# Optimization experiments

Hardware: AMD Instinct MI355X
Metric: run time of the kernel (lower is better)

The kernel has to match this reference:

```python
import jax, jax.numpy as jnp
import numpy as np

N_NODES = 100000
N_EDGES = 3200000
F_IN, F_HID, F_OUT = 32, 32, 16


def spline_conv(x, edge_index, edge_attr, W, root, bias):
    """SplineConv, dim=1, kernel_size=2, degree=1, open spline, aggr='mean'.
    Basis weights over the 2 kernel slots are (1-u, u) for pseudo u in [0,1).
    W: [2, Fin, Fout], root: [Fin, Fout], bias: [Fout]."""
    src, dst = edge_index[0], edge_index[1]
    u = jnp.clip(edge_attr[:, 0:1], 0.0, 1.0)          # [E,1]
    x_src = x[src]                                      # [E,Fin] gather
    msg = (1.0 - u) * (x_src @ W[0]) + u * (x_src @ W[1])  # [E,Fout]
    agg = jax.ops.segment_sum(msg, dst, num_segments=x.shape[0])
    cnt = jax.ops.segment_sum(jnp.ones((msg.shape[0],), dtype=x.dtype), dst,
                              num_segments=x.shape[0])
    agg = agg / jnp.maximum(cnt, 1.0)[:, None]          # mean aggregation
    return agg + x @ root + bias


def setup_inputs() -> dict:
    key = jax.random.key(0)
    ks = jax.random.split(key, 9)
    x = jax.random.normal(ks[0], (N_NODES, F_IN), dtype=jnp.float32)
    edge_index = jax.random.randint(ks[1], (2, N_EDGES), 0, N_NODES, dtype=jnp.int64)
    edge_attr = jax.random.uniform(ks[2], (N_EDGES, 1), dtype=jnp.float32)
    s1 = 1.0 / np.sqrt(F_IN)
    s2 = 1.0 / np.sqrt(F_HID)
    W1 = jax.random.normal(ks[3], (2, F_IN, F_HID), dtype=jnp.float32) * s1
    root1 = jax.random.normal(ks[4], (F_IN, F_HID), dtype=jnp.float32) * s1
    b1 = jnp.zeros((F_HID,), dtype=jnp.float32)
    W2 = jax.random.normal(ks[5], (2, F_HID, F_OUT), dtype=jnp.float32) * s2
    root2 = jax.random.normal(ks[6], (F_HID, F_OUT), dtype=jnp.float32) * s2
    b2 = jnp.zeros((F_OUT,), dtype=jnp.float32)
    return {"x": x, "edge_index": edge_index, "edge_attr": edge_attr,
            "W1": W1, "root1": root1, "b1": b1,
            "W2": W2, "root2": root2, "b2": b2}


def reference(x, edge_index, edge_attr, W1, root1, b1, W2, root2, b2):
    # dropout is identity in eval mode
    h = jax.nn.relu(spline_conv(x, edge_index, edge_attr, W1, root1, b1))
    h = spline_conv(h, edge_index, edge_attr, W2, root2, b2)
    return jax.nn.log_softmax(h, axis=1)
```

## Files before the change

### kernel.cpp

```cpp
#include <hip/hip_runtime.h>
#include <math.h>

#define NN 100000
#define NE 3200000
#define BSH 6
#define BSZ 64
#define NBKT 1563
#define CAP 2560
#define STILE 8192
#define NTBS 391
#define NPB 1563
#define TST 68
#define NOFF (NBKT + 1)

#define FMA4(a, s, v) { (a).x += (s)*(v).x; (a).y += (s)*(v).y; (a).z += (s)*(v).z; (a).w += (s)*(v).w; }

typedef float v2f __attribute__((ext_vector_type(2)));

__device__ __forceinline__ unsigned fp8pack4(float a, float b, float c, float d) {
    int r = __builtin_amdgcn_cvt_pk_fp8_f32(a, b, 0, false);
    r = __builtin_amdgcn_cvt_pk_fp8_f32(c, d, r, true);
    return (unsigned)r;
}

#define LDE(pp, vv, idx) { int e_ = (idx); \
    if (e_ < cn) { pp = (unsigned)pks[cs + e_]; vv = x1[(size_t)(pp >> 15) * 8 + j]; } \
    else { pp = 0u; vv = 0u; } }
#define ACC(pp, vv) { float u_ = (float)((pp) & 511u) * (1.f / 511.f); \
    v2f lo_ = __builtin_amdgcn_cvt_pk_f32_fp8((vv), false); \
    v2f hi_ = __builtin_amdgcn_cvt_pk_f32_fp8((vv), true); \
    T0 += lo_.x; B0 += u_ * lo_.x;  T1 += lo_.y; B1 += u_ * lo_.y; \
    T2 += hi_.x; B2 += u_ * hi_.x;  T3 += hi_.y; B3 += u_ * hi_.y; }

__global__ __launch_bounds__(512) void sp_k(
    const int* __restrict__ ei, const float* __restrict__ ea,
    const float* __restrict__ x, const float* __restrict__ R, const float* __restrict__ b,
    int* __restrict__ pk, unsigned short* __restrict__ offs,
    unsigned* __restrict__ xb, float* __restrict__ xr)
{
    __shared__ __align__(16) union {
        struct { int h[2048]; int staged[STILE]; } sc;
        struct { float Rs[1024]; float xs[64 * 33]; } pp;
    } sm;
    int t = threadIdx.x;

    if (blockIdx.x < NTBS) {
        int* h = sm.sc.h;
        for (int i = t; i < 2048; i += 512) h[i] = 0;
        __syncthreads();
        int e0 = blockIdx.x * STILE;
        int cntblk = NE - e0; if (cntblk > STILE) cntblk = STILE;
        int dreg[16];
        #pragma unroll
        for (int i = 0; i < 16; i++) {
            int e = e0 + i * 512 + t;
            dreg[i] = -1;
            if (e < NE) {
                int d = ei[NE + e];
                dreg[i] = d;
                atomicAdd(&h[d >> BSH], 1);
            }
        }
        __syncthreads();
        int4 hc = ((const int4*)h)[t];
        int s4 = hc.x + hc.y + hc.z + hc.w;
        int lane = t & 63, wv = t >> 6;
        int inc = s4;
        #pragma unroll
        for (int ofs = 1; ofs < 64; ofs <<= 1) {
            int v = __shfl_up(inc, ofs);
            if (lane >= ofs) inc += v;
        }
        int* wsum = sm.sc.staged;
        if (lane == 63) wsum[wv] = inc;
        __syncthreads();
        int base = 0;
        #pragma unroll
        for (int i = 0; i < 8; i++) { int v = wsum[i]; if (i < wv) base += v; }
        int ex = base + inc - s4;
        ((int4*)h)[t] = make_int4(ex, ex + hc.x, ex + hc.x + hc.y, ex + hc.x + hc.y + hc.z);
        __syncthreads();
        for (int k = t; k < NOFF; k += 512)
            offs[(size_t)blockIdx.x * NOFF + k] = (unsigned short)h[k];
        __syncthreads();
        #pragma unroll
        for (int i = 0; i < 16; i++) {
            int d = dreg[i];
            if (d >= 0) {
                int e = e0 + i * 512 + t;
                int src = ei[e];
                float u = fminf(fmaxf(ea[e], 0.f), 1.f);
                unsigned uq = __float2uint_rn(u * 511.f);
                unsigned pck = ((unsigned)src << 15) | ((unsigned)(d & (BSZ - 1)) << 9) | uq;
                int pos = atomicAdd(&h[d >> BSH], 1);
                sm.sc.staged[pos] = (int)pck;
            }
        }
        __syncthreads();
        int* seg = pk + (size_t)blockIdx.x * STILE;
        for (int i = t; i * 4 < cntblk; i += 512)
            ((int4*)seg)[i] = ((const int4*)sm.sc.staged)[i];
    } else {
        for (int i = t; i < 1024; i += 512) sm.pp.Rs[i] = R[i];
        int nb = (blockIdx.x - NTBS) * 64;
        for (int i = t; i < 2048; i += 512) {
            int n = nb + (i >> 5);
            sm.pp.xs[(i >> 5) * 33 + (i & 31)] = (n < NN) ? x[n * 32 + (i & 31)] : 0.f;
        }
        __syncthreads();
        int local = t >> 3, c = t & 7;
        int n = nb + local;
        float4 a2 = make_float4(0.f, 0.f, 0.f, 0.f);
        #pragma unroll
        for (int k = 0; k < 32; k++) {
            float xk = sm.pp.xs[local * 33 + k];
            float4 r = ((const float4*)sm.pp.Rs)[k * 8 + c];
            FMA4(a2, xk, r);
        }
        if (n < NN) {
            float4 bb = ((const float4*)b)[c];
            a2.x += bb.x; a2.y += bb.y; a2.z += bb.z; a2.w += bb.w;
            ((float4*)xr)[n * 8 + c] = a2;
            xb[n * 8 + c] = fp8pack4(sm.pp.xs[local * 33 + c * 4 + 0],
                                     sm.pp.xs[local * 33 + c * 4 + 1],
                                     sm.pp.xs[local * 33 + c * 4 + 2],
                                     sm.pp.xs[local * 33 + c * 4 + 3]);
        }
    }
}

__global__ __launch_bounds__(512, 6) void agg1_k(
    const int* __restrict__ pk, const unsigned short* __restrict__ offs,
    const unsigned* __restrict__ xb, const float* __restrict__ W,
    const float* __restrict__ R2, const float* __restrict__ b2,
    const float* __restrict__ xr, unsigned* __restrict__ hb, float* __restrict__ hr)
{
    __shared__ float Wc[2048];
    __shared__ float R2s[512];
    __shared__ int ccnt[BSZ], coff[BSZ];
    __shared__ int wsum[8];
    __shared__ __align__(16) char smraw[BSZ * TST * 4];
    __shared__ __align__(16) union { int staged[CAP]; float hs[BSZ * 33]; } su;
    int* pks = (int*)smraw;
    float* tb = (float*)smraw;

    int t = threadIdx.x;
    for (int i = t; i < 1024; i += 512) {
        float w0 = W[i];
        Wc[i] = w0;
        Wc[1024 + i] = W[1024 + i] - w0;
    }
    if (t < 512) R2s[t] = R2[t];
    if (t < BSZ) ccnt[t] = 0;

    int bkt = blockIdx.x;
    int cnt = 0, o0 = 0;
    if (t < NTBS) {
        size_t ob = (size_t)t * NOFF + bkt;
        o0 = offs[ob];
        cnt = (int)offs[ob + 1] - o0;
    }
    int lane = t & 63, wv = t >> 6;
    int inc = cnt;
    #pragma unroll
    for (int ofs = 1; ofs < 64; ofs <<= 1) {
        int v = __shfl_up(inc, ofs);
        if (lane >= ofs) inc += v;
    }
    if (lane == 63) wsum[wv] = inc;
    __syncthreads();
    int base = 0, tot = 0;
    #pragma unroll
    for (int i = 0; i < 8; i++) { int v = wsum[i]; tot += v; if (i < wv) base += v; }
    int dst = base + inc - cnt;
    int ne = tot < CAP ? tot : CAP;
    if (dst + cnt > CAP) { cnt = CAP - dst; if (cnt < 0) cnt = 0; }
    const int* seg = pk + (size_t)t * STILE + o0;
    int i2 = 0;
    for (; i2 + 4 <= cnt; i2 += 4) {
        int v0 = seg[i2], v1 = seg[i2 + 1], v2 = seg[i2 + 2], v3 = seg[i2 + 3];
        su.staged[dst + i2] = v0; su.staged[dst + i2 + 1] = v1;
        su.staged[dst + i2 + 2] = v2; su.staged[dst + i2 + 3] = v3;
    }
    for (; i2 < cnt; i2++) su.staged[dst + i2] = seg[i2];
    __syncthreads();

    unsigned er[5]; int rk[5];
    #pragma unroll
    for (int i = 0; i < 5; i++) {
        int e = i * 512 + t;
        rk[i] = -1;
        if (e < ne) {
            er[i] = (unsigned)su.staged[e];
            rk[i] = atomicAdd(&ccnt[(er[i] >> 9) & (BSZ - 1)], 1);
        }
    }
    __syncthreads();
    if (t < BSZ) {
        int v = ccnt[t], sc = v;
        #pragma unroll
        for (int ofs = 1; ofs < 64; ofs <<= 1) {
            int nn = __shfl_up(sc, ofs);
            if (t >= ofs) sc += nn;
        }
        coff[t] = sc - v;
    }
    __syncthreads();
    #pragma unroll
    for (int i = 0; i < 5; i++)
        if (rk[i] >= 0) pks[coff[(er[i] >> 9) & (BSZ - 1)] + rk[i]] = (int)er[i];
    __syncthreads();

    int r = t >> 3, j = t & 7;
    int cs = coff[r], cn = ccnt[r];
    const unsigned* x1 = xb;
    float T0=0,T1=0,T2=0,T3=0,B0=0,B1=0,B2=0,B3=0;
    unsigned pa0, pa1, pa2, pa3, pb0, pb1, pb2, pb3;
    unsigned va0, va1, va2, va3, vb0, vb1, vb2, vb3;
    LDE(pa0, va0, 0) LDE(pa1, va1, 1) LDE(pa2, va2, 2) LDE(pa3, va3, 3)
    LDE(pb0, vb0, 4) LDE(pb1, vb1, 5) LDE(pb2, vb2, 6) LDE(pb3, vb3, 7)
    for (int k = 0; k < cn; k += 8) {
        ACC(pa0, va0) ACC(pa1, va1) ACC(pa2, va2) ACC(pa3, va3)
        LDE(pa0, va0, k + 8)  LDE(pa1, va1, k + 9)  LDE(pa2, va2, k + 10) LDE(pa3, va3, k + 11)
        ACC(pb0, vb0) ACC(pb1, vb1) ACC(pb2, vb2) ACC(pb3, vb3)
        LDE(pb0, vb0, k + 12) LDE(pb1, vb1, k + 13) LDE(pb2, vb2, k + 14) LDE(pb3, vb3, k + 15)
    }
    __syncthreads();

    ((float4*)(tb + r * TST + 4 * j))[0]      = make_float4(T0, T1, T2, T3);
    ((float4*)(tb + r * TST + 32 + 4 * j))[0] = make_float4(B0, B1, B2, B3);
    __syncthreads();

    {
        int row = t >> 3, cc = t & 7;
        int n = bkt * BSZ + row;
        float inv = 1.f / fmaxf((float)ccnt[row], 1.f);
        float4 acc = make_float4(0.f, 0.f, 0.f, 0.f);
        #pragma unroll
        for (int k = 0; k < 32; k++) {
            float sa = tb[row * TST + k];
            float4 w = ((const float4*)Wc)[k * 8 + cc];
            FMA4(acc, sa, w);
        }
        #pragma unroll
        for (int k = 0; k < 32; k++) {
            float sb = tb[row * TST + 32 + k];
            float4 w = ((const float4*)Wc)[(32 + k) * 8 + cc];
            FMA4(acc, sb, w);
        }
        float h0 = 0.f, h1 = 0.f, h2 = 0.f, h3 = 0.f;
        if (n < NN) {
            float4 rr = ((const float4*)xr)[n * 8 + cc];
            h0 = fmaxf(acc.x * inv + rr.x, 0.f);
            h1 = fmaxf(acc.y * inv + rr.y, 0.f);
            h2 = fmaxf(acc.z * inv + rr.z, 0.f);
            h3 = fmaxf(acc.w * inv + rr.w, 0.f);
            hb[n * 8 + cc] = fp8pack4(h0, h1, h2, h3);
        }
        su.hs[row * 33 + cc * 4 + 0] = h0;
        su.hs[row * 33 + cc * 4 + 1] = h1;
        su.hs[row * 33 + cc * 4 + 2] = h2;
        su.hs[row * 33 + cc * 4 + 3] = h3;
    }
    __syncthreads();

    #pragma unroll
    for (int p = 0; p < 2; p++) {
        int idx = p * 512 + t;
        int row = idx >> 4, f = idx & 15;
        int n = bkt * BSZ + row;
        if (n < NN) {
            float o = 0.f;
            #pragma unroll
            for (int k = 0; k < 32; k++) o += su.hs[row * 33 + k] * R2s[k * 16 + f];
            hr[n * 16 + f] = o + b2[f];
        }
    }
}

__global__ __launch_bounds__(512, 6) void agg2_k(
    const int* __restrict__ pk, const unsigned short* __restrict__ offs,
    const unsigned* __restrict__ hb, const float* __restrict__ W,
    const float* __restrict__ hr, float* __restrict__ out)
{
    __shared__ float Wc[1024];
    __shared__ int ccnt[BSZ], coff[BSZ];
    __shared__ int wsum[8];
    __shared__ __align__(16) char smraw[BSZ * TST * 4];
    __shared__ __align__(16) int staged[CAP];
    int* pks = (int*)smraw;
    float* tb = (float*)smraw;

    int t = threadIdx.x;
    if (t < 512) {
        float w0 = W[t];
        Wc[t] = w0;
        Wc[512 + t] = W[512 + t] - w0;
    }
    if (t < BSZ) ccnt[t] = 0;

    int bkt = blockIdx.x;
    int cnt = 0, o0 = 0;
    if (t < NTBS) {
        size_t ob = (size_t)t * NOFF + bkt;
        o0 = offs[ob];
        cnt = (int)offs[ob + 1] - o0;
    }
    int lane = t & 63, wv = t >> 6;
    int inc = cnt;
    #pragma unroll
    for (int ofs = 1; ofs < 64; ofs <<= 1) {
        int v = __shfl_up(inc, ofs);
        if (lane >= ofs) inc += v;
    }
    if (lane == 63) wsum[wv] = inc;
    __syncthreads();
    int base = 0, tot = 0;
    #pragma unroll
    for (int i = 0; i < 8; i++) { int v = wsum[i]; tot += v; if (i < wv) base += v; }
    int dst = base + inc - cnt;
    int ne = tot < CAP ? tot : CAP;
    if (dst + cnt > CAP) { cnt = CAP - dst; if (cnt < 0) cnt = 0; }
    const int* seg = pk + (size_t)t * STILE + o0;
    int i2 = 0;
    for (; i2 + 4 <= cnt; i2 += 4) {
        int v0 = seg[i2], v1 = seg[i2 + 1], v2 = seg[i2 + 2], v3 = seg[i2 + 3];
        staged[dst + i2] = v0; staged[dst + i2 + 1] = v1;
        staged[dst + i2 + 2] = v2; staged[dst + i2 + 3] = v3;
    }
    for (; i2 < cnt; i2++) staged[dst + i2] = seg[i2];
    __syncthreads();

    unsigned er[5]; int rk[5];
    #pragma unroll
    for (int i = 0; i < 5; i++) {
        int e = i * 512 + t;
        rk[i] = -1;
        if (e < ne) {
            er[i] = (unsigned)staged[e];
            rk[i] = atomicAdd(&ccnt[(er[i] >> 9) & (BSZ - 1)], 1);
        }
    }
    __syncthreads();
    if (t < BSZ) {
        int v = ccnt[t], sc = v;
        #pragma unroll
        for (int ofs = 1; ofs < 64; ofs <<= 1) {
            int nn = __shfl_up(sc, ofs);
            if (t >= ofs) sc += nn;
        }
        coff[t] = sc - v;
    }
    __syncthreads();
    #pragma unroll
    for (int i = 0; i < 5; i++)
        if (rk[i] >= 0) pks[coff[(er[i] >> 9) & (BSZ - 1)] + rk[i]] = (int)er[i];
    __syncthreads();

    int r = t >> 3, j = t & 7;
    int cs = coff[r], cn = ccnt[r];
    const unsigned* x1 = hb;
    float T0=0,T1=0,T2=0,T3=0,B0=0,B1=0,B2=0,B3=0;
    unsigned pa0, pa1, pa2, pa3, pb0, pb1, pb2, pb3;
    unsigned va0, va1, va2, va3, vb0, vb1, vb2, vb3;
    LDE(pa0, va0, 0) LDE(pa1, va1, 1) LDE(pa2, va2, 2) LDE(pa3, va3, 3)
    LDE(pb0, vb0, 4) LDE(pb1, vb1, 5) LDE(pb2, vb2, 6) LDE(pb3, vb3, 7)
    for (int k = 0; k < cn; k += 8) {
        ACC(pa0, va0) ACC(pa1, va1) ACC(pa2, va2) ACC(pa3, va3)
        LDE(pa0, va0, k + 8)  LDE(pa1, va1, k + 9)  LDE(pa2, va2, k + 10) LDE(pa3, va3, k + 11)
        ACC(pb0, vb0) ACC(pb1, vb1) ACC(pb2, vb2) ACC(pb3, vb3)
        LDE(pb0, vb0, k + 12) LDE(pb1, vb1, k + 13) LDE(pb2, vb2, k + 14) LDE(pb3, vb3, k + 15)
    }
    __syncthreads();

    ((float4*)(tb + r * TST + 4 * j))[0]      = make_float4(T0, T1, T2, T3);
    ((float4*)(tb + r * TST + 32 + 4 * j))[0] = make_float4(B0, B1, B2, B3);
    __syncthreads();

    #pragma unroll
    for (int p = 0; p < 2; p++) {
        int row = p * 32 + (t >> 4), f = t & 15;
        int n = bkt * BSZ + row;
        float inv = 1.f / fmaxf((float)ccnt[row], 1.f);
        float o = 0.f;
        #pragma unroll
        for (int k = 0; k < 32; k++) o += tb[row * TST + k] * Wc[k * 16 + f];
        #pragma unroll
        for (int k = 0; k < 32; k++) o += tb[row * TST + 32 + k] * Wc[(32 + k) * 16 + f];
        if (n < NN) {
            o = o * inv + hr[n * 16 + f];
            float m = o;
            #pragma unroll
            for (int ofs = 8; ofs; ofs >>= 1) m = fmaxf(m, __shfl_xor(m, ofs, 16));
            float sm = expf(o - m);
            #pragma unroll
            for (int ofs = 8; ofs; ofs >>= 1) sm += __shfl_xor(sm, ofs, 16);
            out[n * 16 + f] = o - (m + logf(sm));
        }
    }
}

extern "C" void kernel_launch(void* const* d_in, const int* in_sizes, int n_in,
                              void* d_out, int out_size, void* d_ws, size_t ws_size,
                              hipStream_t stream) {
    const float* x     = (const float*)d_in[0];
    const int*   ei    = (const int*)d_in[1];
    const float* ea    = (const float*)d_in[2];
    const float* W1    = (const float*)d_in[3];
    const float* root1 = (const float*)d_in[4];
    const float* b1    = (const float*)d_in[5];
    const float* W2    = (const float*)d_in[6];
    const float* root2 = (const float*)d_in[7];
    const float* b2    = (const float*)d_in[8];
    float* out = (float*)d_out;

    int* ws = (int*)d_ws;
    int* pk = ws;
    unsigned short* offs = (unsigned short*)(ws + NE);
    size_t offw = (((size_t)NTBS * NOFF * 2 + 15) / 16) * 4;
    unsigned* xb = (unsigned*)(ws + NE + offw);
    unsigned* hb = xb + (size_t)NN * 8;
    float* xr = (float*)(hb + (size_t)NN * 8);
    float* hr = xr + (size_t)NN * 32;

    sp_k   <<<NTBS + NPB, 512, 0, stream>>>(ei, ea, x, root1, b1, pk, offs, xb, xr);
    agg1_k <<<NBKT, 512, 0, stream>>>(pk, offs, xb, W1, root2, b2, xr, hb, hr);
    agg2_k <<<NBKT, 512, 0, stream>>>(pk, offs, hb, W2, hr, out);
}
```

Before: 237.0 us.

## Transpose bucket offsets, cache sorted edges for layer two, hoist edge loads

A new small kernel transposes the per-tile bucket offset table into a bucket-major packed (offset,count) layout, so the aggregation kernels read it with coalesced loads instead of strided ushort loads. agg1 writes its per-bucket sorted edge list and per-row counts to the workspace, and agg2 reuses them, skipping the gather, scan and local counting sort it used to repeat. The sort kernel now loads src and edge_attr in the first pass, so all global loads are issued before the histogram barrier. The cost is an extra launch, more workspace, extra global writes in agg1, and more live registers in sp_k, whose launch bounds are tightened.

```diff
diff --git a/kernel.cpp b/kernel.cpp
--- a/kernel.cpp
+++ b/kernel.cpp
@@ -12,6 +12,7 @@
 #define NPB 1563
 #define TST 68
 #define NOFF (NBKT + 1)
+#define OS2W 392
 
 #define FMA4(a, s, v) { (a).x += (s)*(v).x; (a).y += (s)*(v).y; (a).z += (s)*(v).z; (a).w += (s)*(v).w; }
 
@@ -32,7 +33,7 @@
     T0 += lo_.x; B0 += u_ * lo_.x;  T1 += lo_.y; B1 += u_ * lo_.y; \
     T2 += hi_.x; B2 += u_ * hi_.x;  T3 += hi_.y; B3 += u_ * hi_.y; }
 
-__global__ __launch_bounds__(512) void sp_k(
+__global__ __launch_bounds__(512, 6) void sp_k(
     const int* __restrict__ ei, const float* __restrict__ ea,
     const float* __restrict__ x, const float* __restrict__ R, const float* __restrict__ b,
     int* __restrict__ pk, unsigned short* __restrict__ offs,
@@ -50,15 +51,19 @@
         __syncthreads();
         int e0 = blockIdx.x * STILE;
         int cntblk = NE - e0; if (cntblk > STILE) cntblk = STILE;
-        int dreg[16];
+        unsigned pck[16]; int bk[16];
         #pragma unroll
         for (int i = 0; i < 16; i++) {
             int e = e0 + i * 512 + t;
-            dreg[i] = -1;
+            bk[i] = -1;
             if (e < NE) {
+                int s = ei[e];
                 int d = ei[NE + e];
-                dreg[i] = d;
-                atomicAdd(&h[d >> BSH], 1);
+                float u = fminf(fmaxf(ea[e], 0.f), 1.f);
+                unsigned uq = __float2uint_rn(u * 511.f);
+                bk[i] = d >> BSH;
+                pck[i] = ((unsigned)s << 15) | ((unsigned)(d & (BSZ - 1)) << 9) | uq;
+                atomicAdd(&h[bk[i]], 1);
             }
         }
         __syncthreads();
@@ -85,15 +90,9 @@
         __syncthreads();
         #pragma unroll
         for (int i = 0; i < 16; i++) {
-            int d = dreg[i];
-            if (d >= 0) {
-                int e = e0 + i * 512 + t;
-                int src = ei[e];
-                float u = fminf(fmaxf(ea[e], 0.f), 1.f);
-                unsigned uq = __float2uint_rn(u * 511.f);
-                unsigned pck = ((unsigned)src << 15) | ((unsigned)(d & (BSZ - 1)) << 9) | uq;
-                int pos = atomicAdd(&h[d >> BSH], 1);
-                sm.sc.staged[pos] = (int)pck;
+            if (bk[i] >= 0) {
+                int pos = atomicAdd(&h[bk[i]], 1);
+                sm.sc.staged[pos] = (int)pck[i];
             }
         }
         __syncthreads();
@@ -129,11 +128,36 @@
     }
 }
 
+__global__ __launch_bounds__(256) void tr_k(
+    const unsigned short* __restrict__ offs, unsigned* __restrict__ offs2)
+{
+    __shared__ unsigned short st[64][68];
+    int kt = blockIdx.x % 25;
+    int tt = blockIdx.x / 25;
+    int t = threadIdx.x;
+    for (int i = t; i < 64 * 66; i += 256) {
+        int r = i / 66, c = i % 66;
+        int row = tt * 64 + r, k = kt * 64 + c;
+        st[r][c] = (row < NTBS && k < NOFF) ? offs[(size_t)row * NOFF + k] : (unsigned short)0;
+    }
+    __syncthreads();
+    for (int i = t; i < 64 * 64; i += 256) {
+        int kl = i >> 6, tl = i & 63;
+        int k = kt * 64 + kl, row = tt * 64 + tl;
+        if (k < NBKT && row < NTBS) {
+            unsigned o0 = st[tl][kl];
+            unsigned cnt = (unsigned)st[tl][kl + 1] - o0;
+            offs2[(size_t)k * OS2W + row] = o0 | (cnt << 16);
+        }
+    }
+}
+
 __global__ __launch_bounds__(512, 6) void agg1_k(
-    const int* __restrict__ pk, const unsigned short* __restrict__ offs,
+    const int* __restrict__ pk, const unsigned* __restrict__ offs2,
     const unsigned* __restrict__ xb, const float* __restrict__ W,
     const float* __restrict__ R2, const float* __restrict__ b2,
-    const float* __restrict__ xr, unsigned* __restrict__ hb, float* __restrict__ hr)
+    const float* __restrict__ xr, unsigned* __restrict__ hb, float* __restrict__ hr,
+    int* __restrict__ pk2, int* __restrict__ cnt2)
 {
     __shared__ float Wc[2048];
     __shared__ float R2s[512];
@@ -156,9 +180,9 @@
     int bkt = blockIdx.x;
     int cnt = 0, o0 = 0;
     if (t < NTBS) {
-        size_t ob = (size_t)t * NOFF + bkt;
-        o0 = offs[ob];
-        cnt = (int)offs[ob + 1] - o0;
+        unsigned pc = offs2[(size_t)bkt * OS2W + t];
+        o0 = (int)(pc & 0xFFFFu);
+        cnt = (int)(pc >> 16);
     }
     int lane = t & 63, wv = t >> 6;
     int inc = cnt;
@@ -209,7 +233,14 @@
     #pragma unroll
     for (int i = 0; i < 5; i++)
         if (rk[i] >= 0) pks[coff[(er[i] >> 9) & (BSZ - 1)] + rk[i]] = (int)er[i];
-    __syncthreads();
+    if (t < BSZ) cnt2[bkt * BSZ + t] = ccnt[t];
+    __syncthreads();
+
+    {
+        int n4 = (ne + 3) >> 2;
+        int4* dp = (int4*)(pk2 + (size_t)bkt * CAP);
+        for (int i = t; i < n4; i += 512) dp[i] = ((const int4*)pks)[i];
+    }
 
     int r = t >> 3, j = t & 7;
     int cs = coff[r], cn = ccnt[r];
@@ -278,16 +309,15 @@
     }
 }
 
-__global__ __launch_bounds__(512, 6) void agg2_k(
-    const int* __restrict__ pk, const unsigned short* __restrict__ offs,
+__global__ __launch_bounds__(512, 8) void agg2_k(
+    const int* __restrict__ pk2, const int* __restrict__ cnt2,
     const unsigned* __restrict__ hb, const float* __restrict__ W,
     const float* __restrict__ hr, float* __restrict__ out)
 {
     __shared__ float Wc[1024];
     __shared__ int ccnt[BSZ], coff[BSZ];
-    __shared__ int wsum[8];
+    __shared__ int smne;
     __shared__ __align__(16) char smraw[BSZ * TST * 4];
-    __shared__ __align__(16) int staged[CAP];
     int* pks = (int*)smraw;
     float* tb = (float*)smraw;
 
@@ -297,64 +327,26 @@
         Wc[t] = w0;
         Wc[512 + t] = W[512 + t] - w0;
     }
-    if (t < BSZ) ccnt[t] = 0;
-
     int bkt = blockIdx.x;
-    int cnt = 0, o0 = 0;
-    if (t < NTBS) {
-        size_t ob = (size_t)t * NOFF + bkt;
-        o0 = offs[ob];
-        cnt = (int)offs[ob + 1] - o0;
-    }
-    int lane = t & 63, wv = t >> 6;
-    int inc = cnt;
-    #pragma unroll
-    for (int ofs = 1; ofs < 64; ofs <<= 1) {
-        int v = __shfl_up(inc, ofs);
-        if (lane >= ofs) inc += v;
-    }
-    if (lane == 63) wsum[wv] = inc;
-    __syncthreads();
-    int base = 0, tot = 0;
-    #pragma unroll
-    for (int i = 0; i < 8; i++) { int v = wsum[i]; tot += v; if (i < wv) base += v; }
-    int dst = base + inc - cnt;
-    int ne = tot < CAP ? tot : CAP;
-    if (dst + cnt > CAP) { cnt = CAP - dst; if (cnt < 0) cnt = 0; }
-    const int* seg = pk + (size_t)t * STILE + o0;
-    int i2 = 0;
-    for (; i2 + 4 <= cnt; i2 += 4) {
-        int v0 = seg[i2], v1 = seg[i2 + 1], v2 = seg[i2 + 2], v3 = seg[i2 + 3];
-        staged[dst + i2] = v0; staged[dst + i2 + 1] = v1;
-        staged[dst + i2 + 2] = v2; staged[dst + i2 + 3] = v3;
-    }
-    for (; i2 < cnt; i2++) staged[dst + i2] = seg[i2];
-    __syncthreads();
-
-    unsigned er[5]; int rk[5];
-    #pragma unroll
-    for (int i = 0; i < 5; i++) {
-        int e = i * 512 + t;
-        rk[i] = -1;
-        if (e < ne) {
-            er[i] = (unsigned)staged[e];
-            rk[i] = atomicAdd(&ccnt[(er[i] >> 9) & (BSZ - 1)], 1);
-        }
-    }
-    __syncthreads();
     if (t < BSZ) {
-        int v = ccnt[t], sc = v;
+        int v = cnt2[bkt * BSZ + t];
+        ccnt[t] = v;
+        int sc = v;
         #pragma unroll
         for (int ofs = 1; ofs < 64; ofs <<= 1) {
             int nn = __shfl_up(sc, ofs);
             if (t >= ofs) sc += nn;
         }
         coff[t] = sc - v;
-    }
-    __syncthreads();
-    #pragma unroll
-    for (int i = 0; i < 5; i++)
-        if (rk[i] >= 0) pks[coff[(er[i] >> 9) & (BSZ - 1)] + rk[i]] = (int)er[i];
+        if (t == 63) smne = sc;
+    }
+    __syncthreads();
+    int ne = smne; if (ne > CAP) ne = CAP;
+    {
+        int n4 = (ne + 3) >> 2;
+        const int4* sp4 = (const int4*)(pk2 + (size_t)bkt * CAP);
+        for (int i = t; i < n4; i += 512) ((int4*)pks)[i] = sp4[i];
+    }
     __syncthreads();
 
     int r = t >> 3, j = t & 7;
@@ -416,14 +408,26 @@
 
     int* ws = (int*)d_ws;
     int* pk = ws;
-    unsigned short* offs = (unsigned short*)(ws + NE);
-    size_t offw = (((size_t)NTBS * NOFF * 2 + 15) / 16) * 4;
-    unsigned* xb = (unsigned*)(ws + NE + offw);
-    unsigned* hb = xb + (size_t)NN * 8;
-    float* xr = (float*)(hb + (size_t)NN * 8);
-    float* hr = xr + (size_t)NN * 32;
+    size_t o_offs  = NE;
+    size_t o_offs2 = o_offs + 305764;
+    size_t o_pk2   = o_offs2 + (size_t)NBKT * OS2W;
+    size_t o_cnt2  = o_pk2 + (size_t)NBKT * CAP;
+    size_t o_xb    = o_cnt2 + (size_t)NBKT * BSZ;
+    size_t o_hb    = o_xb + (size_t)NN * 8;
+    size_t o_xr    = o_hb + (size_t)NN * 8;
+    size_t o_hr    = o_xr + (size_t)NN * 32;
+
+    unsigned short* offs = (unsigned short*)(ws + o_offs);
+    unsigned* offs2 = (unsigned*)(ws + o_offs2);
+    int* pk2 = ws + o_pk2;
+    int* cnt2 = ws + o_cnt2;
+    unsigned* xb = (unsigned*)(ws + o_xb);
+    unsigned* hb = (unsigned*)(ws + o_hb);
+    float* xr = (float*)(ws + o_xr);
+    float* hr = (float*)(ws + o_hr);
 
     sp_k   <<<NTBS + NPB, 512, 0, stream>>>(ei, ea, x, root1, b1, pk, offs, xb, xr);
-    agg1_k <<<NBKT, 512, 0, stream>>>(pk, offs, xb, W1, root2, b2, xr, hb, hr);
-    agg2_k <<<NBKT, 512, 0, stream>>>(pk, offs, hb, W2, hr, out);
-}
+    tr_k   <<<25 * 7, 256, 0, stream>>>(offs, offs2);
+    agg1_k <<<NBKT, 512, 0, stream>>>(pk, offs2, xb, W1, root2, b2, xr, hb, hr, pk2, cnt2);
+    agg2_k <<<NBKT, 512, 0, stream>>>(pk2, cnt2, hb, W2, hr, out);
+}
```

Result: faster. 226.6 us (-4.4%).
